# Performance work log

Measured on AMD Instinct MI355X. Metric: run time of the kernel, lower is better.

Reference implementation:

```python
import jax, jax.numpy as jnp
from jax import lax
import numpy as np

N_CLUSTERS = 8
G_CLUSTERS = 2
D_DIM = 512
DN = ('NCHW', 'OIHW', 'NCHW')


def _conv(x, w, b):
    y = lax.conv_general_dilated(x, w, window_strides=(1, 1), padding='VALID',
                                 dimension_numbers=DN)
    return y + b[None, :, None, None]


def setup_inputs() -> dict:
    key = jax.random.key(0)
    ks = jax.random.split(key, 6)
    B, D, H, W = 32, D_DIM, 7, 250
    KG = N_CLUSTERS + G_CLUSTERS
    scale = 1.0 / np.sqrt(D * 7)
    return {
        'x': jax.random.normal(ks[0], (B, D, H, W), dtype=jnp.float32),
        'feat_w': jax.random.normal(ks[1], (D, D, 7, 1), dtype=jnp.float32) * scale,
        'feat_b': jax.random.normal(ks[2], (D,), dtype=jnp.float32) * 0.01,
        'assign_w': jax.random.normal(ks[3], (KG, D, 7, 1), dtype=jnp.float32) * scale,
        'assign_b': jax.random.normal(ks[4], (KG,), dtype=jnp.float32) * 0.01,
        'centroids': jax.random.uniform(ks[5], (D, KG), dtype=jnp.float32),
    }


def reference(x, feat_w, feat_b, assign_w, assign_b, centroids):
    # features branch: conv(7,1) + ReLU -> (B, D, H', W)
    feat = jnp.maximum(_conv(x, feat_w, feat_b), 0.0)
    # assignment branch: conv(7,1) -> softmax over clusters -> (B, K+G, H', W)
    soft = jax.nn.softmax(_conv(x, assign_w, assign_b), axis=1)
    # Fused VLAD aggregation (mathematically identical to
    # sum_hw soft[b,k,hw] * (feat[b,d,hw] - centroids[d,k]) without
    # materializing the (B,D,K+G,H',W) residual tensor):
    s_sum = soft.sum(axis=(-2, -1))                                # (B, K+G)
    agg = jnp.einsum('bkhw,bdhw->bdk', soft, feat)                 # (B, D, K+G)
    cluster_res = agg - centroids[None, :, :] * s_sum[:, None, :]  # (B, D, K+G)
    cluster_res = cluster_res[..., :N_CLUSTERS]                    # drop ghost clusters
    # L2 normalize over feature dim (torch F.normalize, eps=1e-12)
    norm = jnp.sqrt(jnp.sum(cluster_res * cluster_res, axis=1, keepdims=True))
    cluster_l2 = cluster_res / jnp.maximum(norm, 1e-12)
    # (B, D, K) -> (B, K, D) -> (B, K*D)
    out = jnp.swapaxes(cluster_l2, 1, 2).reshape(x.shape[0], N_CLUSTERS * D_DIM)
    return out
```

## Files before the change

### kernel.cpp

```cpp
#include <hip/hip_runtime.h>
#include <stdint.h>

typedef float f32x4 __attribute__((ext_vector_type(4)));
typedef __bf16 bf16x8 __attribute__((ext_vector_type(8)));
typedef unsigned short ushortx8 __attribute__((ext_vector_type(8)));

#define D_DIM 512
#define KGC 10
#define NCLU 8
#define BATCH 32
#define WPOS 250
#define WPAD 256
#define KDIM 3584
#define MROWS 522
#define MPAD 528
#define MBIG 640
#define BM 160
#define BN 128
#define KSPLIT 2
#define KCHUNK 1792
#define NS 28
#define NT 64
#define KSG 56
#define XTILE 8192

__device__ __forceinline__ float bf2f(unsigned short u) {
  union { unsigned int i; float f; } v; v.i = ((unsigned int)u) << 16; return v.f;
}
__device__ __forceinline__ unsigned short f2bf(float f) {
  union { float f; unsigned int i; } v; v.f = f;
  unsigned int r = v.i + 0x7FFFu + ((v.i >> 16) & 1u);
  return (unsigned short)(r >> 16);
}

__device__ __forceinline__ void load_lds16(const void* g, void* l) {
  __builtin_amdgcn_global_load_lds(
      (const __attribute__((address_space(1))) void*)g,
      (__attribute__((address_space(3))) void*)l, 16, 0, 0);
}

__global__ __launch_bounds__(256) void prep2_kernel(
    const float* __restrict__ fw, const float* __restrict__ fb,
    const float* __restrict__ aw, const float* __restrict__ ab,
    const float* __restrict__ x,
    unsigned short* __restrict__ Wcat, float* __restrict__ bcat,
    unsigned short* __restrict__ XS) {
  const int bid = blockIdx.x;
  const int tid = threadIdx.x;
  if (bid < MBIG) {
    int r = bid;
    unsigned short* dst = Wcat + (size_t)r * KDIM;
    const float* src = (r < D_DIM) ? (fw + (size_t)r * KDIM)
                     : (r < MROWS) ? (aw + (size_t)(r - D_DIM) * KDIM)
                                   : nullptr;
    for (int i = tid; i < KDIM / 4; i += 256) {
      unsigned short o0 = 0, o1 = 0, o2 = 0, o3 = 0;
      if (src) {
        float4 v = ((const float4*)src)[i];
        o0 = f2bf(v.x); o1 = f2bf(v.y); o2 = f2bf(v.z); o3 = f2bf(v.w);
      }
      ushort4 o; o.x = o0; o.y = o1; o.z = o2; o.w = o3;
      ((ushort4*)dst)[i] = o;
    }
    if (tid == 0)
      bcat[r] = r < D_DIM ? fb[r] : (r < MROWS ? ab[r - D_DIM] : 0.f);
  } else {
    const int xt = bid - MBIG;
    const int nt = xt / KSG, ksg = xt - nt * KSG;
    unsigned short* tb = XS + (size_t)(nt * KSG + ksg) * XTILE;
#pragma unroll
    for (int i = 0; i < 4; i++) {
      const int L = tid + 256 * i;
      const int ks = L >> 9, nf = (L >> 6) & 7, lane = L & 63;
      const int fr = lane & 15, kg = lane >> 4;
      const int n = nt * 128 + nf * 16 + fr;
      const int b = n >> 8, col = n & 255;
      const int k0 = ksg * 64 + ks * 32 + kg * 8;
      const float* xp = x + ((size_t)b * KDIM + k0) * WPOS + col;
      ushortx8 pk;
      if (col < WPOS) {
#pragma unroll
        for (int e = 0; e < 8; e++) pk[e] = f2bf(xp[(size_t)e * WPOS]);
      } else {
#pragma unroll
        for (int e = 0; e < 8; e++) pk[e] = 0;
      }
      *(ushortx8*)&tb[(size_t)L * 8] = pk;
    }
  }
}

__global__ __launch_bounds__(512, 4) void gemm_fused(
    const unsigned short* __restrict__ XS, const unsigned short* __restrict__ Wcat,
    float* __restrict__ P) {
  __shared__ __align__(16) unsigned short Wl[2][BM * 64];
  const int tid = threadIdx.x;
  const int nt = blockIdx.x, mh = blockIdx.y, sp = blockIdx.z;
  const int lane = tid & 63, wv = tid >> 6;
  const int wm = wv >> 2, wn = wv & 3;
  const int fr = lane & 15, kg = lane >> 4;
  const int sx = fr & 7;
  const unsigned short* Wg = Wcat + (size_t)mh * BM * KDIM + sp * KCHUNK;
  const unsigned short* xsb = XS + (size_t)nt * (KSG * XTILE)
                                 + (size_t)sp * NS * XTILE
                                 + (wn * 1024 + lane * 8);

  auto stageW = [&](int st, int buf) {
#pragma unroll
    for (int it = 0; it < 3; it++) {
      int s = it * 512 + tid;
      if (s < BM * 8) {
        int row = s >> 3, p = s & 7;
        int blk = p ^ (row & 7);
        load_lds16(Wg + (size_t)row * KDIM + st * 64 + blk * 8, &Wl[buf][s * 8]);
      }
    }
  };
  auto loadX = [&](int st, bf16x8& x0, bf16x8& x1, bf16x8& x2, bf16x8& x3) {
    const unsigned short* p = xsb + (size_t)st * XTILE;
    x0 = *(const bf16x8*)(p);
    x1 = *(const bf16x8*)(p + 512);
    x2 = *(const bf16x8*)(p + 4096);
    x3 = *(const bf16x8*)(p + 4096 + 512);
  };

  f32x4 acc[5][2];
  const f32x4 zero = {0.f, 0.f, 0.f, 0.f};
#pragma unroll
  for (int f = 0; f < 5; f++) { acc[f][0] = zero; acc[f][1] = zero; }

  auto compute = [&](const unsigned short* wb, bf16x8 xa, bf16x8 xb,
                     bf16x8 xc, bf16x8 xd) {
#pragma unroll
    for (int ks = 0; ks < 2; ks++) {
      bf16x8 b0 = ks ? xc : xa;
      bf16x8 b1 = ks ? xd : xb;
      const int off = ((ks * 4 + kg) ^ sx) * 8;
#pragma unroll
      for (int f = 0; f < 5; f++) {
        bf16x8 af = *(const bf16x8*)&wb[(wm * 80 + f * 16 + fr) * 64 + off];
        acc[f][0] = __builtin_amdgcn_mfma_f32_16x16x32_bf16(af, b0, acc[f][0], 0, 0, 0);
        acc[f][1] = __builtin_amdgcn_mfma_f32_16x16x32_bf16(af, b1, acc[f][1], 0, 0, 0);
      }
    }
  };

  bf16x8 xA0, xA1, xA2, xA3, xB0, xB1, xB2, xB3;

  stageW(0, 0);
  loadX(0, xA0, xA1, xA2, xA3);
  __syncthreads();

  for (int t = 0; t < NS; t += 2) {
    stageW(t + 1, 1);
    loadX(t + 1, xB0, xB1, xB2, xB3);
    compute(Wl[0], xA0, xA1, xA2, xA3);
    __syncthreads();
    if (t + 2 < NS) {
      stageW(t + 2, 0);
      loadX(t + 2, xA0, xA1, xA2, xA3);
    }
    compute(Wl[1], xB0, xB1, xB2, xB3);
    __syncthreads();
  }

  float* Pb = P + (size_t)((sp * 4 + mh) * NT + nt) * (BM * BN);
#pragma unroll
  for (int f = 0; f < 5; f++) {
    const int m = wm * 80 + f * 16 + kg * 4;
#pragma unroll
    for (int nf = 0; nf < 2; nf++) {
      const int n = wn * 32 + nf * 16 + fr;
#pragma unroll
      for (int r = 0; r < 4; r++)
        Pb[(size_t)(m + r) * BN + n] = acc[f][nf][r];
    }
  }
}

__global__ __launch_bounds__(256) void reduce_kernel(
    const float* __restrict__ P, const float* __restrict__ bcat,
    unsigned short* __restrict__ Y) {
  const int nt = blockIdx.x, mg = blockIdx.y;
  const int t = threadIdx.x;
  const int m = mg * 16 + (t >> 4);
  const int nl = (t & 15) * 8;
  if (m >= MPAD) return;
  const int mh = (m >= 480) ? 3 : (m >= 320) ? 2 : (m >= 160) ? 1 : 0;
  const int ml = m - mh * BM;
  const size_t slice = (size_t)BM * BN;
  const size_t base = (size_t)ml * BN + nl;
  float s[8];
#pragma unroll
  for (int e = 0; e < 8; e++) s[e] = 0.f;
#pragma unroll
  for (int sp = 0; sp < KSPLIT; sp++) {
    const float* p = P + ((size_t)((sp * 4 + mh) * NT) + nt) * slice + base;
    float4 a = *(const float4*)p;
    float4 c = *(const float4*)(p + 4);
    s[0] += a.x; s[1] += a.y; s[2] += a.z; s[3] += a.w;
    s[4] += c.x; s[5] += c.y; s[6] += c.z; s[7] += c.w;
  }
  float bias = bcat[m];
  ushortx8 o;
#pragma unroll
  for (int e = 0; e < 8; e++) {
    float v = s[e] + bias;
    if (m < D_DIM) v = fmaxf(v, 0.f);
    o[e] = f2bf(v);
  }
  const int nglob = nt * BN + nl;
  const int bb = nglob >> 8, col = nglob & 255;
  *(ushortx8*)&Y[(size_t)bb * MPAD * WPAD + (size_t)m * WPAD + col] = o;
}

__global__ __launch_bounds__(512) void epi_kernel(
    const unsigned short* __restrict__ Y, const float* __restrict__ cent,
    float* __restrict__ out) {
  __shared__ float soft[WPAD];
  __shared__ float red[8];
  const int b = blockIdx.x >> 3, k = blockIdx.x & 7;
  const int tid = threadIdx.x;
  const unsigned short* Yb = Y + (size_t)b * MPAD * WPAD;

  float sv = 0.f;
  if (tid < WPOS) {
    float lg[KGC];
    float mx = -1e30f;
#pragma unroll
    for (int j = 0; j < KGC; j++) {
      lg[j] = bf2f(Yb[(size_t)(D_DIM + j) * WPAD + tid]);
      mx = fmaxf(mx, lg[j]);
    }
    float s = 0.f, ek = 0.f;
#pragma unroll
    for (int j = 0; j < KGC; j++) {
      float e = __expf(lg[j] - mx);
      s += e;
      if (j == k) ek = e;
    }
    sv = ek / s;
  }
  if (tid < WPAD) soft[tid] = sv;
  __syncthreads();

  float v = sv;
#pragma unroll
  for (int o = 32; o > 0; o >>= 1) v += __shfl_down(v, o, 64);
  if ((tid & 63) == 0) red[tid >> 6] = v;
  __syncthreads();
  float ssum = 0.f;
#pragma unroll
  for (int i = 0; i < 8; i++) ssum += red[i];

  float a[8];
#pragma unroll
  for (int u = 0; u < 8; u++) a[u] = 0.f;
  const unsigned short* row = Yb + (size_t)tid * WPAD;
  for (int w = 0; w < WPAD; w += 8) {
    ushortx8 f0 = *(const ushortx8*)(row + w);
    float4 s0 = *(const float4*)&soft[w];
    float4 s1 = *(const float4*)&soft[w + 4];
    a[0] += bf2f(f0[0]) * s0.x;
    a[1] += bf2f(f0[1]) * s0.y;
    a[2] += bf2f(f0[2]) * s0.z;
    a[3] += bf2f(f0[3]) * s0.w;
    a[4] += bf2f(f0[4]) * s1.x;
    a[5] += bf2f(f0[5]) * s1.y;
    a[6] += bf2f(f0[6]) * s1.z;
    a[7] += bf2f(f0[7]) * s1.w;
  }
  float asum = ((a[0] + a[1]) + (a[2] + a[3])) + ((a[4] + a[5]) + (a[6] + a[7]));
  float c = asum - cent[(size_t)tid * KGC + k] * ssum;

  __syncthreads();
  float q = c * c;
#pragma unroll
  for (int o = 32; o > 0; o >>= 1) q += __shfl_down(q, o, 64);
  if ((tid & 63) == 0) red[tid >> 6] = q;
  __syncthreads();
  float nsum = 0.f;
#pragma unroll
  for (int i = 0; i < 8; i++) nsum += red[i];
  float norm = sqrtf(nsum);
  float inv = 1.f / fmaxf(norm, 1e-12f);

  float* ob = out + (size_t)b * (NCLU * D_DIM) + (size_t)k * D_DIM;
  ob[tid] = c * inv;
}

extern "C" void kernel_launch(void* const* d_in, const int* in_sizes, int n_in,
                              void* d_out, int out_size, void* d_ws, size_t ws_size,
                              hipStream_t stream) {
  const float* x  = (const float*)d_in[0];
  const float* fw = (const float*)d_in[1];
  const float* fb = (const float*)d_in[2];
  const float* aw = (const float*)d_in[3];
  const float* ab = (const float*)d_in[4];
  const float* ce = (const float*)d_in[5];
  float* out = (float*)d_out;
  char* ws = (char*)d_ws;

  const size_t WC_BYTES = (size_t)MBIG * KDIM * 2;
  const size_t BC_BYTES = 4096;
  const size_t P_BYTES  = (size_t)KSPLIT * 4 * NT * BM * BN * 4;
  const size_t XS_BYTES = (size_t)NT * KSG * XTILE * 2;
  unsigned short* Wc = (unsigned short*)(ws);
  float*          bc = (float*)(ws + WC_BYTES);
  float*          P  = (float*)(ws + WC_BYTES + BC_BYTES);
  unsigned short* XSp= (unsigned short*)(ws + WC_BYTES + BC_BYTES + P_BYTES);
  unsigned short* Yv = XSp;

  prep2_kernel<<<MBIG + NT * KSG, 256, 0, stream>>>(fw, fb, aw, ab, x, Wc, bc, XSp);
  gemm_fused<<<dim3(NT, 4, KSPLIT), 512, 0, stream>>>(XSp, Wc, P);
  reduce_kernel<<<dim3(NT, 40), 256, 0, stream>>>(P, bc, Yv);
  epi_kernel<<<BATCH * NCLU, 512, 0, stream>>>(Yv, ce, out);
}
```

Measured before the change: 250.8 us.

## Drop split-K, fuse bias/ReLU epilogue into GEMM, deepen W pipeline to four buffers

Removes the two-way K split and the separate reduce kernel. The GEMM now runs the full K range and writes bf16 output with bias and ReLU applied directly. The weight staging moves to a four-slot LDS ring with explicit vmcnt waits and raw barriers, so loads run two stages ahead. This avoids the fp32 partial-sum round trip through global memory and one kernel launch, but halves the grid to 256 blocks. Occupancy drops to two blocks per CU and the epilogue stores become scattered 2-byte writes.

Result: no change. 255.0 us (+1.7%).

```diff
diff --git a/kernel.cpp b/kernel.cpp
--- a/kernel.cpp
+++ b/kernel.cpp
@@ -17,9 +17,7 @@
 #define MBIG 640
 #define BM 160
 #define BN 128
-#define KSPLIT 2
-#define KCHUNK 1792
-#define NS 28
+#define NS 56
 #define NT 64
 #define KSG 56
 #define XTILE 8192
@@ -90,30 +88,26 @@
   }
 }
 
-__global__ __launch_bounds__(512, 4) void gemm_fused(
+__global__ __launch_bounds__(512, 2) void gemm_fused(
     const unsigned short* __restrict__ XS, const unsigned short* __restrict__ Wcat,
-    float* __restrict__ P) {
-  __shared__ __align__(16) unsigned short Wl[2][BM * 64];
+    const float* __restrict__ bcat, unsigned short* __restrict__ Y) {
+  __shared__ __align__(16) unsigned short Wl[4][BM * 64];
   const int tid = threadIdx.x;
-  const int nt = blockIdx.x, mh = blockIdx.y, sp = blockIdx.z;
+  const int nt = blockIdx.x, mh = blockIdx.y;
   const int lane = tid & 63, wv = tid >> 6;
   const int wm = wv >> 2, wn = wv & 3;
   const int fr = lane & 15, kg = lane >> 4;
   const int sx = fr & 7;
-  const unsigned short* Wg = Wcat + (size_t)mh * BM * KDIM + sp * KCHUNK;
-  const unsigned short* xsb = XS + (size_t)nt * (KSG * XTILE)
-                                 + (size_t)sp * NS * XTILE
-                                 + (wn * 1024 + lane * 8);
+  const unsigned short* Wg = Wcat + (size_t)mh * BM * KDIM;
+  const unsigned short* xsb = XS + (size_t)nt * (KSG * XTILE) + (wn * 1024 + lane * 8);
 
   auto stageW = [&](int st, int buf) {
 #pragma unroll
     for (int it = 0; it < 3; it++) {
-      int s = it * 512 + tid;
-      if (s < BM * 8) {
-        int row = s >> 3, p = s & 7;
-        int blk = p ^ (row & 7);
-        load_lds16(Wg + (size_t)row * KDIM + st * 64 + blk * 8, &Wl[buf][s * 8]);
-      }
+      int s = (it < 2) ? it * 512 + tid : 1024 + (tid & 255);
+      int row = s >> 3, p = s & 7;
+      int blk = p ^ (row & 7);
+      load_lds16(Wg + (size_t)row * KDIM + st * 64 + blk * 8, &Wl[buf][s * 8]);
     }
   };
   auto loadX = [&](int st, bf16x8& x0, bf16x8& x1, bf16x8& x2, bf16x8& x3) {
@@ -129,12 +123,12 @@
 #pragma unroll
   for (int f = 0; f < 5; f++) { acc[f][0] = zero; acc[f][1] = zero; }
 
-  auto compute = [&](const unsigned short* wb, bf16x8 xa, bf16x8 xb,
-                     bf16x8 xc, bf16x8 xd) {
+  auto compute = [&](const unsigned short* wb, bf16x8 b00, bf16x8 b01,
+                     bf16x8 b10, bf16x8 b11) {
 #pragma unroll
     for (int ks = 0; ks < 2; ks++) {
-      bf16x8 b0 = ks ? xc : xa;
-      bf16x8 b1 = ks ? xd : xb;
+      bf16x8 b0 = ks ? b10 : b00;
+      bf16x8 b1 = ks ? b11 : b01;
       const int off = ((ks * 4 + kg) ^ sx) * 8;
 #pragma unroll
       for (int f = 0; f < 5; f++) {
@@ -146,72 +140,52 @@
   };
 
   bf16x8 xA0, xA1, xA2, xA3, xB0, xB1, xB2, xB3;
-
-  stageW(0, 0);
-  loadX(0, xA0, xA1, xA2, xA3);
-  __syncthreads();
-
-  for (int t = 0; t < NS; t += 2) {
-    stageW(t + 1, 1);
-    loadX(t + 1, xB0, xB1, xB2, xB3);
-    compute(Wl[0], xA0, xA1, xA2, xA3);
-    __syncthreads();
-    if (t + 2 < NS) {
-      stageW(t + 2, 0);
-      loadX(t + 2, xA0, xA1, xA2, xA3);
-    }
-    compute(Wl[1], xB0, xB1, xB2, xB3);
-    __syncthreads();
-  }
-
-  float* Pb = P + (size_t)((sp * 4 + mh) * NT + nt) * (BM * BN);
+  bf16x8 xC0, xC1, xC2, xC3, xD0, xD1, xD2, xD3;
+
+  stageW(0, 0); loadX(0, xA0, xA1, xA2, xA3);
+  stageW(1, 1); loadX(1, xB0, xB1, xB2, xB3);
+
+#define STEP(u, BUF, PBUF, CX0, CX1, CX2, CX3, PX0, PX1, PX2, PX3)           \
+  {                                                                          \
+    if ((u) + 1 < NS) { asm volatile("s_waitcnt vmcnt(7)" ::: "memory"); }   \
+    else              { asm volatile("s_waitcnt vmcnt(0)" ::: "memory"); }   \
+    __builtin_amdgcn_s_barrier();                                            \
+    __builtin_amdgcn_sched_barrier(0);                                       \
+    if ((u) + 2 < NS) {                                                      \
+      stageW((u) + 2, PBUF);                                                 \
+      loadX((u) + 2, PX0, PX1, PX2, PX3);                                    \
+    }                                                                        \
+    compute(Wl[BUF], CX0, CX1, CX2, CX3);                                    \
+  }
+
+  for (int t = 0; t < NS; t += 4) {
+    STEP(t + 0, 0, 2, xA0, xA1, xA2, xA3, xC0, xC1, xC2, xC3);
+    STEP(t + 1, 1, 3, xB0, xB1, xB2, xB3, xD0, xD1, xD2, xD3);
+    STEP(t + 2, 2, 0, xC0, xC1, xC2, xC3, xA0, xA1, xA2, xA3);
+    STEP(t + 3, 3, 1, xD0, xD1, xD2, xD3, xB0, xB1, xB2, xB3);
+  }
+#undef STEP
+
+  const int bb = (nt * BN) >> 8;
+  const int cbase = (nt * BN) & 255;
+  unsigned short* Yb = Y + (size_t)bb * MPAD * WPAD;
 #pragma unroll
   for (int f = 0; f < 5; f++) {
-    const int m = wm * 80 + f * 16 + kg * 4;
+    const int m0 = mh * BM + wm * 80 + f * 16 + kg * 4;
 #pragma unroll
     for (int nf = 0; nf < 2; nf++) {
-      const int n = wn * 32 + nf * 16 + fr;
-#pragma unroll
-      for (int r = 0; r < 4; r++)
-        Pb[(size_t)(m + r) * BN + n] = acc[f][nf][r];
-    }
-  }
-}
-
-__global__ __launch_bounds__(256) void reduce_kernel(
-    const float* __restrict__ P, const float* __restrict__ bcat,
-    unsigned short* __restrict__ Y) {
-  const int nt = blockIdx.x, mg = blockIdx.y;
-  const int t = threadIdx.x;
-  const int m = mg * 16 + (t >> 4);
-  const int nl = (t & 15) * 8;
-  if (m >= MPAD) return;
-  const int mh = (m >= 480) ? 3 : (m >= 320) ? 2 : (m >= 160) ? 1 : 0;
-  const int ml = m - mh * BM;
-  const size_t slice = (size_t)BM * BN;
-  const size_t base = (size_t)ml * BN + nl;
-  float s[8];
-#pragma unroll
-  for (int e = 0; e < 8; e++) s[e] = 0.f;
-#pragma unroll
-  for (int sp = 0; sp < KSPLIT; sp++) {
-    const float* p = P + ((size_t)((sp * 4 + mh) * NT) + nt) * slice + base;
-    float4 a = *(const float4*)p;
-    float4 c = *(const float4*)(p + 4);
-    s[0] += a.x; s[1] += a.y; s[2] += a.z; s[3] += a.w;
-    s[4] += c.x; s[5] += c.y; s[6] += c.z; s[7] += c.w;
-  }
-  float bias = bcat[m];
-  ushortx8 o;
-#pragma unroll
-  for (int e = 0; e < 8; e++) {
-    float v = s[e] + bias;
-    if (m < D_DIM) v = fmaxf(v, 0.f);
-    o[e] = f2bf(v);
-  }
-  const int nglob = nt * BN + nl;
-  const int bb = nglob >> 8, col = nglob & 255;
-  *(ushortx8*)&Y[(size_t)bb * MPAD * WPAD + (size_t)m * WPAD + col] = o;
+      const int c = cbase + wn * 32 + nf * 16 + fr;
+#pragma unroll
+      for (int r = 0; r < 4; r++) {
+        const int m = m0 + r;
+        if (m < MPAD) {
+          float v = acc[f][nf][r] + bcat[m];
+          if (m < D_DIM) v = fmaxf(v, 0.f);
+          Yb[(size_t)m * WPAD + c] = f2bf(v);
+        }
+      }
+    }
+  }
 }
 
 __global__ __launch_bounds__(512) void epi_kernel(
@@ -303,16 +277,13 @@
 
   const size_t WC_BYTES = (size_t)MBIG * KDIM * 2;
   const size_t BC_BYTES = 4096;
-  const size_t P_BYTES  = (size_t)KSPLIT * 4 * NT * BM * BN * 4;
   const size_t XS_BYTES = (size_t)NT * KSG * XTILE * 2;
   unsigned short* Wc = (unsigned short*)(ws);
   float*          bc = (float*)(ws + WC_BYTES);
-  float*          P  = (float*)(ws + WC_BYTES + BC_BYTES);
-  unsigned short* XSp= (unsigned short*)(ws + WC_BYTES + BC_BYTES + P_BYTES);
-  unsigned short* Yv = XSp;
+  unsigned short* XSp= (unsigned short*)(ws + WC_BYTES + BC_BYTES);
+  unsigned short* Yv = (unsigned short*)(ws + WC_BYTES + BC_BYTES + XS_BYTES);
 
   prep2_kernel<<<MBIG + NT * KSG, 256, 0, stream>>>(fw, fb, aw, ab, x, Wc, bc, XSp);
-  gemm_fused<<<dim3(NT, 4, KSPLIT), 512, 0, stream>>>(XSp, Wc, P);
-  reduce_kernel<<<dim3(NT, 40), 256, 0, stream>>>(P, bc, Yv);
+  gemm_fused<<<dim3(NT, 4), 512, 0, stream>>>(XSp, Wc, bc, Yv);
   epi_kernel<<<BATCH * NCLU, 512, 0, stream>>>(Yv, ce, out);
 }
```
